# Optimization experiments

Hardware: AMD Instinct MI355X
Metric: run time of the kernel (lower is better)

The kernel has to match this reference:

```python
import jax, jax.numpy as jnp
import numpy as np

NGRAM = 16
SUB = 512  # bytes per sub-block


def byte2image(block, ngram=NGRAM):
    """block: (B, L) int -> (B, 1, ngram*8, L-ngram) float32 in [-1, 1]."""
    B, L = block.shape
    blk = block.astype(jnp.int32)
    # nxt[:, i] = blk[:, i+1], last column zero
    nxt = jnp.concatenate([blk[:, 1:], jnp.zeros((B, 1), jnp.int32)], axis=1)
    # 8 bit-shifted views of the byte stream
    shifts = jnp.stack(
        [((blk << s) & 255) + ((nxt >> (8 - s)) & 255) for s in range(8)],
        axis=1,
    )  # (B, 8, L)
    flat = shifts.reshape(B, -1)  # (B, 8*L)
    parts = [flat] + [jnp.roll(flat, -i, axis=1) for i in range(1, ngram)]
    stacked = jnp.concatenate(parts, axis=1).reshape(B, ngram * 8, L)
    result = stacked[:, :, :-ngram].astype(jnp.float32)
    result = (result / 255.0 - 0.5) / 0.5
    return result[:, None]  # (B, 1, ngram*8, L-ngram)


def byte2image_4k(block, ngram=NGRAM):
    """block: (B, 4096) -> (B, 8, ngram*8, 512-ngram)."""
    return jnp.concatenate(
        [byte2image(block[:, i * SUB:(i + 1) * SUB], ngram) for i in range(8)],
        axis=1,
    )


def setup_inputs() -> dict:
    key = jax.random.key(0)
    kx, kw = jax.random.split(key)
    x = jax.random.randint(kx, (256, 4096), 0, 256, dtype=jnp.int64)
    W = jax.random.normal(kw, (496, 64), dtype=jnp.float32) * 0.02
    return {"x": x, "W": W}


def reference(x, W):
    # ByteFormerWrapper.forward with block_size=4096: byte2image_4k then the
    # (opaque) model; model stood in by a linear head over the image width.
    img = byte2image_4k(x)                      # (B, 8, 128, 496)
    out = jnp.einsum('bchw,wo->bcho', img, W)   # (B, 8, 128, 64)
    return out
```

## Files before the change

### kernel.cpp

```cpp
#include <hip/hip_runtime.h>

typedef unsigned short u16;
typedef unsigned int u32;
typedef _Float16 half8 __attribute__((ext_vector_type(8)));
typedef __attribute__((ext_vector_type(4))) float floatx4;

#define LSTRIDE 72
#define BIMG (128 * LSTRIDE)

__device__ __forceinline__ void gl_lds16(const void* g, void* l) {
  __builtin_amdgcn_global_load_lds(
      (const __attribute__((address_space(1))) void*)g,
      (__attribute__((address_space(3))) void*)l, 16, 0, 0);
}
__device__ __forceinline__ void gl_lds4(const void* g, void* l) {
  __builtin_amdgcn_global_load_lds(
      (const __attribute__((address_space(1))) void*)g,
      (__attribute__((address_space(3))) void*)l, 4, 0, 0);
}

__global__ __launch_bounds__(256) void byteformer_precompute(
    const float* __restrict__ Wm, u16* __restrict__ Bws,
    float* __restrict__ csumWs) {
  const int t = threadIdx.x;
  const int y = blockIdx.x >> 3, kc = blockIdx.x & 7;
  const int wave = t >> 6, o = t & 63;
  const int pp = wave >> 1, hf = wave & 1;
  u16* img = Bws + (size_t)blockIdx.x * BIMG;
  #pragma unroll
  for (int i = 0; i < 18; ++i) {
    const int kk = (hf * 18 + i) * 2;
    u32 val = 0u;
    if (kk < 64) {
      const int c0 = kc * 64 + kk - 2 * y - pp;
      const int c1 = c0 + 1;
      float f0 = (c0 >= 0 && c0 < 496) ? Wm[c0 * 64 + o] : 0.0f;
      float f1 = (c1 >= 0 && c1 < 496) ? Wm[c1 * 64 + o] : 0.0f;
      u16 h0 = __builtin_bit_cast(unsigned short, (_Float16)f0);
      u16 h1 = __builtin_bit_cast(unsigned short, (_Float16)f1);
      val = (u32)h0 | ((u32)h1 << 16);
    }
    *(u32*)&img[(pp * 64 + o) * LSTRIDE + kk] = val;
  }
  if (blockIdx.x == 0) {
    __shared__ float red[256];
    float s = 0.0f;
    for (int c = wave * 124; c < wave * 124 + 124; ++c) s += Wm[c * 64 + o];
    red[t] = s;
    __syncthreads();
    if (t < 64)
      csumWs[t] = (1024.0f * (2.0f / 255.0f) + 1.0f) *
                  (red[t] + red[t + 64] + red[t + 128] + red[t + 192]);
  }
}

__global__ __launch_bounds__(256, 2) void byteformer_fused(
    const int* __restrict__ x, const u16* __restrict__ Bws,
    const float* __restrict__ csumWs, float* __restrict__ out) {
  __shared__ __align__(16) u16 arena[4 * BIMG];

  const int t = threadIdx.x;
  const int mtile = blockIdx.x;
  const int y = blockIdx.y;

  const int wave = t >> 6, lane = t & 63;
  const int wm = wave >> 1, wn = wave & 1;
  const int quad = lane >> 4, l16 = lane & 15;

  const int sA_sub = t >> 4;
  const int sA_kg  = (t >> 1) & 7;
  const int sA_qh  = t & 1;
  const long xrow = ((long)mtile * 16 + sA_sub) * 512;
  const char* bimg0 = (const char*)(Bws + (size_t)y * 8 * BIMG);

  floatx4 acc[4][4];
  #pragma unroll
  for (int mt = 0; mt < 4; ++mt)
    #pragma unroll
    for (int nt = 0; nt < 4; ++nt)
      acc[mt][nt] = floatx4{0.f, 0.f, 0.f, 0.f};

  float cs[4];
  #pragma unroll
  for (int nt = 0; nt < 4; ++nt) cs[nt] = csumWs[nt * 16 + l16];

  int4 ca, cb; int cc;
  auto xload = [&](int kc) {
    const int base = kc * 64 + sA_kg * 8;
    ca = *(const int4*)&x[xrow + base];
    cb = *(const int4*)&x[xrow + base + 4];
    cc = (base + 8 < 512) ? x[xrow + base + 8] : 0;
  };

  auto bdma = [&](int kc, u16* dstb) {
    const char* src = bimg0 + (size_t)kc * 18432;
    char* dst = (char*)dstb;
    const int woff = wave * 1024;
    #pragma unroll
    for (int j = 0; j < 4; ++j)
      gl_lds16(src + j * 4096 + woff + lane * 16, dst + j * 4096 + woff);
    const int woff4 = 16384 + wave * 256;
    #pragma unroll
    for (int j = 0; j < 2; ++j)
      gl_lds4(src + woff4 + j * 1024 + lane * 4, dst + woff4 + j * 1024);
  };

  auto astage = [&](u16* dstb) {
    const u32 c0 = (u32)ca.x, c1 = (u32)ca.y, c2 = (u32)ca.z, c3 = (u32)ca.w;
    const u32 c4 = (u32)cb.x, c5 = (u32)cb.y, c6 = (u32)cb.z, c7 = (u32)cb.w;
    const u32 c8 = (u32)cc;
    const u32 P0 = ((c0 << 8) | c1) | (((c1 << 8) | c2) << 16);
    const u32 P1 = ((c2 << 8) | c3) | (((c3 << 8) | c4) << 16);
    const u32 P2 = ((c4 << 8) | c5) | (((c5 << 8) | c6) << 16);
    const u32 P3 = ((c6 << 8) | c7) | (((c7 << 8) | c8) << 16);
    u16* arow = &dstb[(sA_sub * 8 + sA_qh * 4) * LSTRIDE + sA_kg * 8];
    #pragma unroll
    for (int qi = 0; qi < 4; ++qi) {
      const int sh = 8 - (sA_qh * 4 + qi);
      int4 d;
      d.x = (int)(((P0 >> sh) & 0x00FF00FFu) | 0x64006400u);
      d.y = (int)(((P1 >> sh) & 0x00FF00FFu) | 0x64006400u);
      d.z = (int)(((P2 >> sh) & 0x00FF00FFu) | 0x64006400u);
      d.w = (int)(((P3 >> sh) & 0x00FF00FFu) | 0x64006400u);
      *(int4*)(arow + qi * LSTRIDE) = d;
    }
  };

  auto compute = [&](const u16* Ab, const u16* Bb) {
    #pragma unroll
    for (int ks = 0; ks < 2; ++ks) {
      const int koff = ks * 32 + quad * 8;
      half8 af[4], bf[4];
      #pragma unroll
      for (int mt = 0; mt < 4; ++mt)
        af[mt] = *(const half8*)&Ab[(wm * 64 + mt * 16 + l16) * LSTRIDE + koff];
      #pragma unroll
      for (int nt = 0; nt < 4; ++nt)
        bf[nt] = *(const half8*)&Bb[(wn * 64 + nt * 16 + l16) * LSTRIDE + koff];
      #pragma unroll
      for (int mt = 0; mt < 4; ++mt)
        #pragma unroll
        for (int nt = 0; nt < 4; ++nt)
          acc[mt][nt] = __builtin_amdgcn_mfma_f32_16x16x32_f16(
              af[mt], bf[nt], acc[mt][nt], 0, 0, 0);
    }
  };

  bdma(0, arena + 2 * BIMG);
  xload(0);
  astage(arena);
  __syncthreads();

  #pragma unroll
  for (int kc = 0; kc < 8; ++kc) {
    u16* Acur = arena + (kc & 1) * BIMG;
    u16* Bcur = arena + (2 + (kc & 1)) * BIMG;
    u16* Anxt = arena + ((kc + 1) & 1) * BIMG;
    u16* Bnxt = arena + (2 + ((kc + 1) & 1)) * BIMG;
    if (kc < 7) {
      xload(kc + 1);
      bdma(kc + 1, Bnxt);
    }
    compute(Acur, Bcur);
    if (kc < 7) astage(Anxt);
    __syncthreads();
  }

  float* ep = (float*)arena;
  const float S = 2.0f / 255.0f;
  #pragma unroll
  for (int mt = 0; mt < 4; ++mt) {
    #pragma unroll
    for (int i = 0; i < 4; ++i) {
      const int mr = wm * 64 + mt * 16 + quad * 4 + i;
      const int sub_l = mr >> 3, q = mr & 7;
      const int rowbase = sub_l * 1040 + wn * 512 + q * 64 + l16;
      #pragma unroll
      for (int nt = 0; nt < 4; ++nt)
        ep[rowbase + nt * 16] = S * acc[mt][nt][i] - cs[nt];
    }
  }
  __syncthreads();

  const long outbase = (long)mtile * 16 * 8192 + (long)y * 1024;
  #pragma unroll
  for (int k2 = 0; k2 < 16; ++k2) {
    const float4 v =
        *(const float4*)((const char*)ep + k2 * 4160 + wave * 1024 + lane * 16);
    *(float4*)&out[outbase + (long)k2 * 8192 + wave * 256 + lane * 4] = v;
  }
}

extern "C" void kernel_launch(void* const* d_in, const int* in_sizes, int n_in,
                              void* d_out, int out_size, void* d_ws, size_t ws_size,
                              hipStream_t stream) {
  const int* x = (const int*)d_in[0];
  const float* Wm = (const float*)d_in[1];
  float* out = (float*)d_out;
  u16* Bws = (u16*)d_ws;
  float* csumWs = (float*)((char*)d_ws + (size_t)64 * BIMG * 2);
  byteformer_precompute<<<dim3(64), dim3(256), 0, stream>>>(Wm, Bws, csumWs);
  byteformer_fused<<<dim3(128, 8), dim3(256), 0, stream>>>(x, Bws, csumWs, out);
}
```

Measured before the change: 119.5 us.

## Fuse weight preprocessing into main kernel, build shifted fp16 B tiles in-register

Removes the separate precompute kernel that wrote shifted fp16 weight images and column sums to workspace. Each block now loads fp32 W rows directly, converts them to fp16 and writes the shifted B tiles to LDS itself, and it accumulates the column sum locally with a block reduction. This saves a kernel launch and the workspace round trip. In exchange every block redoes the conversion work, holds 17 extra registers, and issues scalar global loads instead of async global-to-LDS DMA.

```diff
diff --git a/kernel.cpp b/kernel.cpp
--- a/kernel.cpp
+++ b/kernel.cpp
@@ -8,56 +8,12 @@
 #define LSTRIDE 72
 #define BIMG (128 * LSTRIDE)
 
-__device__ __forceinline__ void gl_lds16(const void* g, void* l) {
-  __builtin_amdgcn_global_load_lds(
-      (const __attribute__((address_space(1))) void*)g,
-      (__attribute__((address_space(3))) void*)l, 16, 0, 0);
-}
-__device__ __forceinline__ void gl_lds4(const void* g, void* l) {
-  __builtin_amdgcn_global_load_lds(
-      (const __attribute__((address_space(1))) void*)g,
-      (__attribute__((address_space(3))) void*)l, 4, 0, 0);
-}
-
-__global__ __launch_bounds__(256) void byteformer_precompute(
-    const float* __restrict__ Wm, u16* __restrict__ Bws,
-    float* __restrict__ csumWs) {
-  const int t = threadIdx.x;
-  const int y = blockIdx.x >> 3, kc = blockIdx.x & 7;
-  const int wave = t >> 6, o = t & 63;
-  const int pp = wave >> 1, hf = wave & 1;
-  u16* img = Bws + (size_t)blockIdx.x * BIMG;
-  #pragma unroll
-  for (int i = 0; i < 18; ++i) {
-    const int kk = (hf * 18 + i) * 2;
-    u32 val = 0u;
-    if (kk < 64) {
-      const int c0 = kc * 64 + kk - 2 * y - pp;
-      const int c1 = c0 + 1;
-      float f0 = (c0 >= 0 && c0 < 496) ? Wm[c0 * 64 + o] : 0.0f;
-      float f1 = (c1 >= 0 && c1 < 496) ? Wm[c1 * 64 + o] : 0.0f;
-      u16 h0 = __builtin_bit_cast(unsigned short, (_Float16)f0);
-      u16 h1 = __builtin_bit_cast(unsigned short, (_Float16)f1);
-      val = (u32)h0 | ((u32)h1 << 16);
-    }
-    *(u32*)&img[(pp * 64 + o) * LSTRIDE + kk] = val;
-  }
-  if (blockIdx.x == 0) {
-    __shared__ float red[256];
-    float s = 0.0f;
-    for (int c = wave * 124; c < wave * 124 + 124; ++c) s += Wm[c * 64 + o];
-    red[t] = s;
-    __syncthreads();
-    if (t < 64)
-      csumWs[t] = (1024.0f * (2.0f / 255.0f) + 1.0f) *
-                  (red[t] + red[t + 64] + red[t + 128] + red[t + 192]);
-  }
-}
-
 __global__ __launch_bounds__(256, 2) void byteformer_fused(
-    const int* __restrict__ x, const u16* __restrict__ Bws,
-    const float* __restrict__ csumWs, float* __restrict__ out) {
+    const int* __restrict__ x, const float* __restrict__ Wm,
+    float* __restrict__ out) {
   __shared__ __align__(16) u16 arena[4 * BIMG];
+  __shared__ float part[256];
+  __shared__ float csumsh[64];
 
   const int t = threadIdx.x;
   const int mtile = blockIdx.x;
@@ -71,7 +27,6 @@
   const int sA_kg  = (t >> 1) & 7;
   const int sA_qh  = t & 1;
   const long xrow = ((long)mtile * 16 + sA_sub) * 512;
-  const char* bimg0 = (const char*)(Bws + (size_t)y * 8 * BIMG);
 
   floatx4 acc[4][4];
   #pragma unroll
@@ -80,11 +35,11 @@
     for (int nt = 0; nt < 4; ++nt)
       acc[mt][nt] = floatx4{0.f, 0.f, 0.f, 0.f};
 
-  float cs[4];
-  #pragma unroll
-  for (int nt = 0; nt < 4; ++nt) cs[nt] = csumWs[nt * 16 + l16];
+  float csum_local = 0.0f;
 
   int4 ca, cb; int cc;
+  float f[17];
+
   auto xload = [&](int kc) {
     const int base = kc * 64 + sA_kg * 8;
     ca = *(const int4*)&x[xrow + base];
@@ -92,17 +47,13 @@
     cc = (base + 8 < 512) ? x[xrow + base + 8] : 0;
   };
 
-  auto bdma = [&](int kc, u16* dstb) {
-    const char* src = bimg0 + (size_t)kc * 18432;
-    char* dst = (char*)dstb;
-    const int woff = wave * 1024;
+  auto wload = [&](int kc) {
+    const int cbase = kc * 64 + 16 * wave - 2 * y - 1;
     #pragma unroll
-    for (int j = 0; j < 4; ++j)
-      gl_lds16(src + j * 4096 + woff + lane * 16, dst + j * 4096 + woff);
-    const int woff4 = 16384 + wave * 256;
-    #pragma unroll
-    for (int j = 0; j < 2; ++j)
-      gl_lds4(src + woff4 + j * 1024 + lane * 4, dst + woff4 + j * 1024);
+    for (int j = 0; j < 17; ++j) {
+      const int c = cbase + j;
+      f[j] = (c >= 0 && c < 496) ? Wm[c * 64 + lane] : 0.0f;
+    }
   };
 
   auto astage = [&](u16* dstb) {
@@ -126,6 +77,29 @@
     }
   };
 
+  auto bstage = [&](u16* dstb) {
+    u16 h[17];
+    #pragma unroll
+    for (int j = 0; j < 17; ++j)
+      h[j] = __builtin_bit_cast(unsigned short, (_Float16)f[j]);
+    #pragma unroll
+    for (int j = 1; j <= 16; ++j) csum_local += f[j];
+    #pragma unroll
+    for (int g = 0; g < 2; ++g) {
+      const int mgrp = 2 * wave + g;
+      #pragma unroll
+      for (int pp = 0; pp < 2; ++pp) {
+        const int jb = g * 8 + 1 - pp;
+        int4 d;
+        d.x = (int)((u32)h[jb + 0] | ((u32)h[jb + 1] << 16));
+        d.y = (int)((u32)h[jb + 2] | ((u32)h[jb + 3] << 16));
+        d.z = (int)((u32)h[jb + 4] | ((u32)h[jb + 5] << 16));
+        d.w = (int)((u32)h[jb + 6] | ((u32)h[jb + 7] << 16));
+        *(int4*)&dstb[(pp * 64 + lane) * LSTRIDE + mgrp * 8] = d;
+      }
+    }
+  };
+
   auto compute = [&](const u16* Ab, const u16* Bb) {
     #pragma unroll
     for (int ks = 0; ks < 2; ++ks) {
@@ -146,9 +120,8 @@
     }
   };
 
-  bdma(0, arena + 2 * BIMG);
-  xload(0);
-  astage(arena);
+  xload(0); wload(0);
+  astage(arena); bstage(arena + 2 * BIMG);
   __syncthreads();
 
   #pragma unroll
@@ -157,17 +130,25 @@
     u16* Bcur = arena + (2 + (kc & 1)) * BIMG;
     u16* Anxt = arena + ((kc + 1) & 1) * BIMG;
     u16* Bnxt = arena + (2 + ((kc + 1) & 1)) * BIMG;
-    if (kc < 7) {
-      xload(kc + 1);
-      bdma(kc + 1, Bnxt);
-    }
+    if (kc < 7) { xload(kc + 1); wload(kc + 1); }
     compute(Acur, Bcur);
-    if (kc < 7) astage(Anxt);
+    if (kc < 7) { astage(Anxt); bstage(Bnxt); }
     __syncthreads();
   }
 
+  const float S = 2.0f / 255.0f;
+  const float K1 = 1024.0f * S + 1.0f;
+  part[t] = csum_local;
+  __syncthreads();
+  if (t < 64)
+    csumsh[t] = K1 * (part[t] + part[t + 64] + part[t + 128] + part[t + 192]);
+  __syncthreads();
+
+  float cs[4];
+  #pragma unroll
+  for (int nt = 0; nt < 4; ++nt) cs[nt] = csumsh[nt * 16 + l16];
+
   float* ep = (float*)arena;
-  const float S = 2.0f / 255.0f;
   #pragma unroll
   for (int mt = 0; mt < 4; ++mt) {
     #pragma unroll
@@ -197,8 +178,5 @@
   const int* x = (const int*)d_in[0];
   const float* Wm = (const float*)d_in[1];
   float* out = (float*)d_out;
-  u16* Bws = (u16*)d_ws;
-  float* csumWs = (float*)((char*)d_ws + (size_t)64 * BIMG * 2);
-  byteformer_precompute<<<dim3(64), dim3(256), 0, stream>>>(Wm, Bws, csumWs);
-  byteformer_fused<<<dim3(128, 8), dim3(256), 0, stream>>>(x, Bws, csumWs, out);
+  byteformer_fused<<<dim3(128, 8), dim3(256), 0, stream>>>(x, Wm, out);
 }
```

Result: faster. 108.7 us (-9.0%).
